# Kernel tuning notes

Hardware: AMD Instinct MI355X
Metric: run time of the kernel (lower is better)

Reference implementation:

```python
import jax, jax.numpy as jnp
import numpy as np
from jax import lax

E, H, O, T = 1024, 2048, 2, 2048

def setup_inputs() -> dict:
    key = jax.random.key(0)
    ks = jax.random.split(key, 10)
    sc = lambda k, shape: (jax.random.normal(k, shape, dtype=jnp.float32) * 0.02)
    return {
        "h0": jax.random.normal(ks[0], (1, 1, H), dtype=jnp.float32),
        "c0": jax.random.normal(ks[1], (1, 1, H), dtype=jnp.float32),
        "ground_truth": jax.random.normal(ks[2], (1, T, O), dtype=jnp.float32),
        "use_gt": jax.random.randint(ks[3], (T,), 0, 2, dtype=jnp.int32),
        "W_emb": sc(ks[4], (E, O)), "b_emb": jnp.zeros((E,), jnp.float32),
        "W_ih": sc(ks[5], (4 * H, E)), "b_ih": jnp.zeros((4 * H,), jnp.float32),
        "W_hh": sc(ks[6], (4 * H, H)), "b_hh": jnp.zeros((4 * H,), jnp.float32),
        "W_out": sc(ks[7], (O, H)), "b_out": jnp.zeros((O,), jnp.float32),
        "output_length": T,
    }

def reference(h0, c0, ground_truth, use_gt, W_emb, b_emb, W_ih, b_ih, W_hh, b_hh, W_out, b_out, output_length):
    h = h0.reshape(-1)            # [H]
    c = c0.reshape(-1)            # [H]
    gt = ground_truth[0]          # [T, 2]
    # initial input: embedding of ones([1,2])
    x0 = W_emb @ jnp.ones((O,), jnp.float32) + b_emb  # [E]

    def step(carry, inp):
        h, c, x = carry
        gt_t, ug = inp
        gates = W_ih @ x + b_ih + W_hh @ h + b_hh      # [4H], PyTorch gate order i,f,g,o
        i, f, g, o = jnp.split(gates, 4)
        c_new = jax.nn.sigmoid(f) * c + jax.nn.sigmoid(i) * jnp.tanh(g)
        h_new = jax.nn.sigmoid(o) * jnp.tanh(c_new)
        raw = W_out @ h_new + b_out                    # [2]
        loss_t = jnp.mean((raw - gt_t) ** 2)           # MSELoss per step
        nxt = jnp.where(ug == 1, gt_t, raw)            # teacher forcing branch
        x_new = W_emb @ nxt + b_emb
        return (h_new, c_new, x_new), (raw, loss_t)

    (_, _, _), (preds, losses) = lax.scan(
        step, (h, c, x0), (gt[:output_length], use_gt[:output_length]))
    return preds, jnp.sum(losses)
```

## Files before the change

kernel.cpp:

```cpp
#include <hip/hip_runtime.h>

#define NWG   256
#define NTHR  256
#define TT    2048
#define HH    2048
#define EE    1024

__device__ __forceinline__ float wred(float v){
  v += __shfl_xor(v, 1, 64);
  v += __shfl_xor(v, 2, 64);
  v += __shfl_xor(v, 4, 64);
  v += __shfl_xor(v, 8, 64);
  v += __shfl_xor(v, 16, 64);
  v += __shfl_xor(v, 32, 64);
  return v;
}

__device__ __forceinline__ float sigm(float x){ return 1.0f / (1.0f + __expf(-x)); }

extern "C" __global__ void __launch_bounds__(NTHR, 1)
lstm_seq_kernel(const float* __restrict__ h0, const float* __restrict__ c0,
                const float* __restrict__ gt, const int* __restrict__ ugt,
                const float* __restrict__ W_emb, const float* __restrict__ b_emb,
                const float* __restrict__ W_ih, const float* __restrict__ b_ih,
                const float* __restrict__ W_hh, const float* __restrict__ b_hh,
                const float* __restrict__ W_out, const float* __restrict__ b_out,
                float* __restrict__ out, unsigned long long* __restrict__ hbuf)
{
  const int wgid = blockIdx.x;
  const int tid  = threadIdx.x;
  const int gw   = tid >> 6;
  const int l    = tid & 63;
  const int j0   = wgid * 8;
  const int uA   = j0 + 2*gw;

  __shared__ float h_lds[2][HH];

  float2 whh[8][16];
  #pragma unroll
  for (int u = 0; u < 8; ++u){
    const float* rp = W_hh + (size_t)(2048*(u>>1) + uA + (u&1)) * HH;
    #pragma unroll
    for (int i = 0; i < 16; ++i)
      whh[u][i] = *(const float2*)(rp + 2*l + 128*i);
  }
  float2 wo0[16], wo1[16];
  #pragma unroll
  for (int i = 0; i < 16; ++i){
    wo0[i] = *(const float2*)(W_out + 2*l + 128*i);
    wo1[i] = *(const float2*)(W_out + HH + 2*l + 128*i);
  }
  const float bo0 = b_out[0], bo1 = b_out[1];

  float aE0[8], aE1[8], aB[8];
  #pragma unroll
  for (int u = 0; u < 8; ++u){ aE0[u] = 0.f; aE1[u] = 0.f; aB[u] = 0.f; }
  for (int i = 0; i < 16; ++i){
    const int k = l + 64*i;
    const float2 we = *(const float2*)(W_emb + 2*k);
    const float be = b_emb[k];
    #pragma unroll
    for (int u = 0; u < 8; ++u){
      const float wv = W_ih[(size_t)(2048*(u>>1) + uA + (u&1))*EE + k];
      aE0[u] = fmaf(wv, we.x, aE0[u]);
      aE1[u] = fmaf(wv, we.y, aE1[u]);
      aB[u]  = fmaf(wv, be,  aB[u]);
    }
  }
  float e0v[8], e1v[8], bv[8];
  #pragma unroll
  for (int u = 0; u < 8; ++u){
    const int r = 2048*(u>>1) + uA + (u&1);
    e0v[u] = wred(aE0[u]);
    e1v[u] = wred(aE1[u]);
    bv[u]  = wred(aB[u]) + b_ih[r] + b_hh[r];
  }

  float cA = c0[uA], cB = c0[uA + 1];

  for (int t = 0; t < TT; ++t){
    float g0 = 0.f, g1 = 0.f; int ug = 0;
    if (t > 0){
      g0 = gt[2*(t-1)]; g1 = gt[2*(t-1)+1]; ug = ugt[t-1];
    }

    float* hl = h_lds[t & 1];
    const int e0i = (gw << 9) + l;
    if (t == 0){
      #pragma unroll
      for (int i = 0; i < 8; ++i)
        hl[e0i + (i<<6)] = h0[e0i + (i<<6)];
    } else {
      const unsigned long long* bp = hbuf + ((t-1)&1)*HH + e0i;
      const unsigned tagexp = (unsigned)t;
      unsigned fresh = 0; int rounds = 0;
      while (fresh != 0xFFu){
        unsigned long long v[8];
        #pragma unroll
        for (int i = 0; i < 8; ++i)
          v[i] = __hip_atomic_load(bp + (i<<6), __ATOMIC_RELAXED, __HIP_MEMORY_SCOPE_AGENT);
        #pragma unroll
        for (int i = 0; i < 8; ++i){
          if (!(fresh & (1u<<i)) && (unsigned)(v[i] >> 32) == tagexp){
            hl[e0i + (i<<6)] = __uint_as_float((unsigned)v[i]);
            fresh |= (1u<<i);
          }
        }
        if (++rounds > 16384) break;
      }
    }
    __syncthreads();

    float ga[8];
    #pragma unroll
    for (int u = 0; u < 8; ++u) ga[u] = 0.f;
    float r0 = 0.f, r1 = 0.f;
    #pragma unroll
    for (int i = 0; i < 16; ++i){
      const float2 hv = *(const float2*)(hl + 2*l + 128*i);
      r0 = fmaf(wo0[i].x, hv.x, r0); r0 = fmaf(wo0[i].y, hv.y, r0);
      r1 = fmaf(wo1[i].x, hv.x, r1); r1 = fmaf(wo1[i].y, hv.y, r1);
      #pragma unroll
      for (int u = 0; u < 8; ++u){
        ga[u] = fmaf(whh[u][i].x, hv.x, ga[u]);
        ga[u] = fmaf(whh[u][i].y, hv.y, ga[u]);
      }
    }
    #pragma unroll
    for (int u = 0; u < 8; ++u) ga[u] = wred(ga[u]);
    r0 = wred(r0); r1 = wred(r1);

    const float raw0 = r0 + bo0, raw1 = r1 + bo1;
    float n0, n1;
    if (t == 0){ n0 = 1.f; n1 = 1.f; }
    else {
      if (wgid == 0 && tid == 0){
        out[2*(t-1)]   = raw0;
        out[2*(t-1)+1] = raw1;
      }
      n0 = (ug == 1) ? g0 : raw0;
      n1 = (ug == 1) ? g1 : raw1;
    }

    float gf[8];
    #pragma unroll
    for (int u = 0; u < 8; ++u)
      gf[u] = ga[u] + fmaf(e0v[u], n0, fmaf(e1v[u], n1, bv[u]));
    const float cAn = sigm(gf[2])*cA + sigm(gf[0])*tanhf(gf[4]);
    const float hA  = sigm(gf[6])*tanhf(cAn); cA = cAn;
    const float cBn = sigm(gf[3])*cB + sigm(gf[1])*tanhf(gf[5]);
    const float hB  = sigm(gf[7])*tanhf(cBn); cB = cBn;

    if (l < 2){
      const float hv = (l == 0) ? hA : hB;
      const unsigned long long pk =
          ((unsigned long long)(unsigned)(t + 1) << 32) |
          (unsigned long long)__float_as_uint(hv);
      __hip_atomic_store(hbuf + (t&1)*HH + uA + l, pk, __ATOMIC_RELAXED, __HIP_MEMORY_SCOPE_AGENT);
    }
  }

  if (wgid != 0) return;

  {
    float* hl = h_lds[0];
    const int e0i = (gw << 9) + l;
    const unsigned long long* bp = hbuf + ((TT-1)&1)*HH + e0i;
    const unsigned tagexp = (unsigned)TT;
    unsigned fresh = 0; int rounds = 0;
    while (fresh != 0xFFu){
      unsigned long long v[8];
      #pragma unroll
      for (int i = 0; i < 8; ++i)
        v[i] = __hip_atomic_load(bp + (i<<6), __ATOMIC_RELAXED, __HIP_MEMORY_SCOPE_AGENT);
      #pragma unroll
      for (int i = 0; i < 8; ++i){
        if (!(fresh & (1u<<i)) && (unsigned)(v[i] >> 32) == tagexp){
          hl[e0i + (i<<6)] = __uint_as_float((unsigned)v[i]);
          fresh |= (1u<<i);
        }
      }
      if (++rounds > 16384) break;
    }
  }
  __syncthreads();
  if (gw == 0){
    const float* hl = h_lds[0];
    float r0 = 0.f, r1 = 0.f;
    #pragma unroll
    for (int i = 0; i < 16; ++i){
      const float2 hv = *(const float2*)(hl + 2*l + 128*i);
      r0 = fmaf(wo0[i].x, hv.x, r0); r0 = fmaf(wo0[i].y, hv.y, r0);
      r1 = fmaf(wo1[i].x, hv.x, r1); r1 = fmaf(wo1[i].y, hv.y, r1);
    }
    r0 = wred(r0); r1 = wred(r1);
    if (l == 0){
      out[2*(TT-1)]   = r0 + bo0;
      out[2*(TT-1)+1] = r1 + bo1;
    }
  }
}

extern "C" __global__ void loss_kernel(const float* __restrict__ preds,
                                       const float* __restrict__ gt,
                                       float* __restrict__ loss_out)
{
  const int tid = threadIdx.x;
  float acc = 0.f;
  #pragma unroll
  for (int s = 0; s < 8; ++s){
    const int t = tid + 256*s;
    const float d0 = preds[2*t]   - gt[2*t];
    const float d1 = preds[2*t+1] - gt[2*t+1];
    acc += 0.5f*(d0*d0 + d1*d1);
  }
  acc = wred(acc);
  __shared__ float ws[4];
  if ((tid & 63) == 0) ws[tid >> 6] = acc;
  __syncthreads();
  if (tid == 0) loss_out[0] = ws[0] + ws[1] + ws[2] + ws[3];
}

extern "C" void kernel_launch(void* const* d_in, const int* in_sizes, int n_in,
                              void* d_out, int out_size, void* d_ws, size_t ws_size,
                              hipStream_t stream)
{
  (void)in_sizes; (void)n_in; (void)out_size; (void)ws_size;
  const float* h0    = (const float*)d_in[0];
  const float* c0    = (const float*)d_in[1];
  const float* gt    = (const float*)d_in[2];
  const int*   ugt   = (const int*)  d_in[3];
  const float* W_emb = (const float*)d_in[4];
  const float* b_emb = (const float*)d_in[5];
  const float* W_ih  = (const float*)d_in[6];
  const float* b_ih  = (const float*)d_in[7];
  const float* W_hh  = (const float*)d_in[8];
  const float* b_hh  = (const float*)d_in[9];
  const float* W_out = (const float*)d_in[10];
  const float* b_out = (const float*)d_in[11];
  float* out  = (float*)d_out;
  unsigned long long* hbuf = (unsigned long long*)d_ws;

  void* args[] = { &h0, &c0, &gt, &ugt, &W_emb, &b_emb, &W_ih, &b_ih,
                   &W_hh, &b_hh, &W_out, &b_out, &out, &hbuf };
  hipLaunchCooperativeKernel((const void*)lstm_seq_kernel,
                             dim3(NWG), dim3(NTHR), args, 0, stream);

  loss_kernel<<<dim3(1), dim3(NTHR), 0, stream>>>(out, gt, out + 2*TT);
}
```

Baseline: 9.110 ms.

## Consume h directly from global poll buffer, dropping LDS staging and barrier

Each wavefront now polls every tagged h element it needs straight from the global exchange buffer and folds each chunk into the gate and output dot products as soon as its tag matches. This removes the shared-memory staging, the per-step __syncthreads, and the split between waiting and computing, so arithmetic overlaps with waiting for late producers. In exchange, each wave issues four times as many atomic loads per step (the whole 2048-element vector rather than a quarter of it), and the conditional FMA blocks inside the unrolled poll loop may increase register pressure on an already heavily register-resident kernel.

```diff
diff --git a/kernel.cpp b/kernel.cpp
--- a/kernel.cpp
+++ b/kernel.cpp
@@ -34,8 +34,6 @@
   const int j0   = wgid * 8;
   const int uA   = j0 + 2*gw;
 
-  __shared__ float h_lds[2][HH];
-
   float2 whh[8][16];
   #pragma unroll
   for (int u = 0; u < 8; ++u){
@@ -78,54 +76,68 @@
 
   float cA = c0[uA], cB = c0[uA + 1];
 
+#define FMA_CHUNK(i, hv)                                              \
+  do {                                                                \
+    r0 = fmaf(wo0[i].x, (hv).x, r0); r0 = fmaf(wo0[i].y, (hv).y, r0); \
+    r1 = fmaf(wo1[i].x, (hv).x, r1); r1 = fmaf(wo1[i].y, (hv).y, r1); \
+    _Pragma("unroll")                                                 \
+    for (int u = 0; u < 8; ++u){                                      \
+      ga[u] = fmaf(whh[u][i].x, (hv).x, ga[u]);                       \
+      ga[u] = fmaf(whh[u][i].y, (hv).y, ga[u]);                       \
+    }                                                                 \
+  } while (0)
+
   for (int t = 0; t < TT; ++t){
     float g0 = 0.f, g1 = 0.f; int ug = 0;
     if (t > 0){
       g0 = gt[2*(t-1)]; g1 = gt[2*(t-1)+1]; ug = ugt[t-1];
     }
 
-    float* hl = h_lds[t & 1];
-    const int e0i = (gw << 9) + l;
+    float ga[8];
+    #pragma unroll
+    for (int u = 0; u < 8; ++u) ga[u] = 0.f;
+    float r0 = 0.f, r1 = 0.f;
+
     if (t == 0){
       #pragma unroll
-      for (int i = 0; i < 8; ++i)
-        hl[e0i + (i<<6)] = h0[e0i + (i<<6)];
+      for (int i = 0; i < 16; ++i){
+        const float2 hv = *(const float2*)(h0 + 2*l + 128*i);
+        FMA_CHUNK(i, hv);
+      }
     } else {
-      const unsigned long long* bp = hbuf + ((t-1)&1)*HH + e0i;
+      const unsigned long long* bp = hbuf + ((t-1)&1)*HH + 2*l;
       const unsigned tagexp = (unsigned)t;
-      unsigned fresh = 0; int rounds = 0;
-      while (fresh != 0xFFu){
-        unsigned long long v[8];
+      unsigned pend = 0xFFFFu;
+      int rounds = 0;
+      while (pend){
         #pragma unroll
-        for (int i = 0; i < 8; ++i)
-          v[i] = __hip_atomic_load(bp + (i<<6), __ATOMIC_RELAXED, __HIP_MEMORY_SCOPE_AGENT);
-        #pragma unroll
-        for (int i = 0; i < 8; ++i){
-          if (!(fresh & (1u<<i)) && (unsigned)(v[i] >> 32) == tagexp){
-            hl[e0i + (i<<6)] = __uint_as_float((unsigned)v[i]);
-            fresh |= (1u<<i);
+        for (int h8 = 0; h8 < 2; ++h8){
+          unsigned long long va[8], vb[8];
+          #pragma unroll
+          for (int j = 0; j < 8; ++j){
+            const int i = h8*8 + j;
+            if (pend & (1u<<i)){
+              va[j] = __hip_atomic_load(bp + 128*i,     __ATOMIC_RELAXED, __HIP_MEMORY_SCOPE_AGENT);
+              vb[j] = __hip_atomic_load(bp + 128*i + 1, __ATOMIC_RELAXED, __HIP_MEMORY_SCOPE_AGENT);
+            }
+          }
+          #pragma unroll
+          for (int j = 0; j < 8; ++j){
+            const int i = h8*8 + j;
+            if ((pend & (1u<<i)) &&
+                (unsigned)(va[j] >> 32) == tagexp && (unsigned)(vb[j] >> 32) == tagexp){
+              float2 hv;
+              hv.x = __uint_as_float((unsigned)va[j]);
+              hv.y = __uint_as_float((unsigned)vb[j]);
+              FMA_CHUNK(i, hv);
+              pend &= ~(1u<<i);
+            }
           }
         }
-        if (++rounds > 16384) break;
-      }
-    }
-    __syncthreads();
-
-    float ga[8];
-    #pragma unroll
-    for (int u = 0; u < 8; ++u) ga[u] = 0.f;
-    float r0 = 0.f, r1 = 0.f;
-    #pragma unroll
-    for (int i = 0; i < 16; ++i){
-      const float2 hv = *(const float2*)(hl + 2*l + 128*i);
-      r0 = fmaf(wo0[i].x, hv.x, r0); r0 = fmaf(wo0[i].y, hv.y, r0);
-      r1 = fmaf(wo1[i].x, hv.x, r1); r1 = fmaf(wo1[i].y, hv.y, r1);
-      #pragma unroll
-      for (int u = 0; u < 8; ++u){
-        ga[u] = fmaf(whh[u][i].x, hv.x, ga[u]);
-        ga[u] = fmaf(whh[u][i].y, hv.y, ga[u]);
-      }
-    }
+        if (++rounds > 32768) break;
+      }
+    }
+
     #pragma unroll
     for (int u = 0; u < 8; ++u) ga[u] = wred(ga[u]);
     r0 = wred(r0); r1 = wred(r1);
@@ -161,37 +173,28 @@
   }
 
   if (wgid != 0) return;
-
-  {
-    float* hl = h_lds[0];
-    const int e0i = (gw << 9) + l;
-    const unsigned long long* bp = hbuf + ((TT-1)&1)*HH + e0i;
+  if (gw == 0){
+    const unsigned long long* bp = hbuf + ((TT-1)&1)*HH + 2*l;
     const unsigned tagexp = (unsigned)TT;
-    unsigned fresh = 0; int rounds = 0;
-    while (fresh != 0xFFu){
-      unsigned long long v[8];
+    float r0 = 0.f, r1 = 0.f;
+    unsigned pend = 0xFFFFu;
+    int rounds = 0;
+    while (pend){
       #pragma unroll
-      for (int i = 0; i < 8; ++i)
-        v[i] = __hip_atomic_load(bp + (i<<6), __ATOMIC_RELAXED, __HIP_MEMORY_SCOPE_AGENT);
-      #pragma unroll
-      for (int i = 0; i < 8; ++i){
-        if (!(fresh & (1u<<i)) && (unsigned)(v[i] >> 32) == tagexp){
-          hl[e0i + (i<<6)] = __uint_as_float((unsigned)v[i]);
-          fresh |= (1u<<i);
+      for (int i = 0; i < 16; ++i){
+        if (pend & (1u<<i)){
+          const unsigned long long va = __hip_atomic_load(bp + 128*i,     __ATOMIC_RELAXED, __HIP_MEMORY_SCOPE_AGENT);
+          const unsigned long long vb = __hip_atomic_load(bp + 128*i + 1, __ATOMIC_RELAXED, __HIP_MEMORY_SCOPE_AGENT);
+          if ((unsigned)(va >> 32) == tagexp && (unsigned)(vb >> 32) == tagexp){
+            const float hx = __uint_as_float((unsigned)va);
+            const float hy = __uint_as_float((unsigned)vb);
+            r0 = fmaf(wo0[i].x, hx, r0); r0 = fmaf(wo0[i].y, hy, r0);
+            r1 = fmaf(wo1[i].x, hx, r1); r1 = fmaf(wo1[i].y, hy, r1);
+            pend &= ~(1u<<i);
+          }
         }
       }
-      if (++rounds > 16384) break;
-    }
-  }
-  __syncthreads();
-  if (gw == 0){
-    const float* hl = h_lds[0];
-    float r0 = 0.f, r1 = 0.f;
-    #pragma unroll
-    for (int i = 0; i < 16; ++i){
-      const float2 hv = *(const float2*)(hl + 2*l + 128*i);
-      r0 = fmaf(wo0[i].x, hv.x, r0); r0 = fmaf(wo0[i].y, hv.y, r0);
-      r1 = fmaf(wo1[i].x, hv.x, r1); r1 = fmaf(wo1[i].y, hv.y, r1);
+      if (++rounds > 32768) break;
     }
     r0 = wred(r0); r1 = wred(r1);
     if (l == 0){
@@ -199,6 +202,7 @@
       out[2*(TT-1)+1] = r1 + bo1;
     }
   }
+#undef FMA_CHUNK
 }
 
 extern "C" __global__ void loss_kernel(const float* __restrict__ preds,
@@ -246,5 +250,5 @@
   hipLaunchCooperativeKernel((const void*)lstm_seq_kernel,
                              dim3(NWG), dim3(NTHR), args, 0, stream);
 
-  loss_kernel<<<dim3(1), dim3(NTHR), 0, stream>>>(out, gt, out + 2*TT);
-}
+  loss_kernel<<<dim3(1), dim3(256), 0, stream>>>(out, gt, out + 2*TT);
+}
```

New measurement: 21.88 ms. +140.2%, slower.
